# Kernel optimization log

Measured on AMD Instinct MI355X. Metric: run time of the kernel, lower is better.

Reference implementation:

```python
import jax, jax.numpy as jnp
import numpy as np

B, C, L = 16, 256, 2048


def setup_inputs() -> dict:
    key = jax.random.key(0)
    ks = jax.random.split(key, 7)
    s = 0.05
    return {
        "x": jax.random.normal(ks[0], (B, C, L), dtype=jnp.float32),
        "W_theta": jax.random.normal(ks[1], (C, C), dtype=jnp.float32) * s,
        "b_theta": jax.random.normal(ks[2], (C,), dtype=jnp.float32) * s,
        "W_phi": jax.random.normal(ks[3], (C, C), dtype=jnp.float32) * s,
        "b_phi": jax.random.normal(ks[4], (C,), dtype=jnp.float32) * s,
        "W_g": jax.random.normal(ks[5], (C, C), dtype=jnp.float32) * s,
        "b_g": jax.random.normal(ks[6], (C,), dtype=jnp.float32) * s,
    }


def reference(x, W_theta, b_theta, W_phi, b_phi, W_g, b_g):
    # x: [B, C, L]; 1x1 Conv1d == linear over channel dim: out[b,o,l] = W[o,c] x[b,c,l] + b[o]
    q = jnp.einsum('oc,bcl->bol', W_theta, x) + b_theta[None, :, None]  # [B,C,L]
    k = jnp.einsum('oc,bcl->bol', W_phi, x) + b_phi[None, :, None]
    v = jnp.einsum('oc,bcl->bol', W_g, x) + b_g[None, :, None]
    num_c = x.shape[1]
    # scores[b,i,j] = sum_c q[b,c,i] * k[b,c,j]
    scores = jnp.einsum('bci,bcj->bij', q, k) / jnp.sqrt(jnp.float32(num_c))  # [B,L,L]
    attn = jax.nn.softmax(scores, axis=-1)
    # out[b,i,c] = sum_j attn[b,i,j] v[b,c,j]; then permute back to [B,C,L]
    attn_out = jnp.einsum('bij,bcj->bci', attn, v)  # [B,C,L]
    return x + attn_out
```

## Files before the change

kernel.cpp:

```cpp
#include <hip/hip_runtime.h>
#include <math.h>

#define B_ 16
#define C_ 256
#define L_ 2048

using short8 = __attribute__((ext_vector_type(8))) short;
using f32x4  = __attribute__((ext_vector_type(4))) float;
using f32x16 = __attribute__((ext_vector_type(16))) float;
typedef unsigned int uint;

__device__ __forceinline__ unsigned short f2bf(float f) {
  unsigned u = __float_as_uint(f);
  return (unsigned short)((u + 0x7FFFu + ((u >> 16) & 1u)) >> 16);
}

__device__ __forceinline__ void gload16(const void* src, void* dst) {
  __builtin_amdgcn_global_load_lds(
      (const __attribute__((address_space(1))) unsigned int*)src,
      (__attribute__((address_space(3))) unsigned int*)dst, 16, 0, 0);
}

__global__ __launch_bounds__(256) void convert_w(const float* __restrict__ wt,
                                                 const float* __restrict__ wp,
                                                 const float* __restrict__ wg,
                                                 unsigned short* __restrict__ dst) {
  int i = blockIdx.x * 256 + threadIdx.x;
  dst[i]          = f2bf(wt[i]);
  dst[65536 + i]  = f2bf(wp[i]);
  dst[131072 + i] = f2bf(wg[i]);
}

__global__ __launch_bounds__(256, 2) void proj_kernel(
    const float* __restrict__ x, const unsigned short* __restrict__ wbf,
    const float* __restrict__ bth, const float* __restrict__ bph,
    const float* __restrict__ bg,
    unsigned short* __restrict__ qT, unsigned short* __restrict__ kT,
    unsigned short* __restrict__ vv)
{
  const int tid  = threadIdx.x;
  const int w    = tid >> 6;
  const int lane = tid & 63;
  const int r    = lane & 15;
  const int g    = lane >> 4;
  const int l0   = blockIdx.x * 64;
  const int b    = blockIdx.y;
  const int p    = blockIdx.z;

  __shared__ unsigned short xs[64 * 64];
  __shared__ unsigned short wsd[256 * 64];

  const unsigned short* wsrc = wbf + p * 65536;

  f32x4 acc[4][4];
#pragma unroll
  for (int mi = 0; mi < 4; ++mi)
#pragma unroll
    for (int ni = 0; ni < 4; ++ni) acc[mi][ni] = f32x4{0.f, 0.f, 0.f, 0.f};

  for (int ks = 0; ks < 4; ++ks) {
    __syncthreads();
#pragma unroll
    for (int it = 0; it < 8; ++it) {
      int d  = it * 256 + w * 64 + lane;
      int o  = d >> 3;
      int cs = d & 7;
      const unsigned short* src = wsrc + o * C_ + ks * 64 + ((cs ^ (o & 7)) << 3);
      gload16(src, (void*)(wsd + (size_t)(it * 256 + w * 64) * 8));
    }
#pragma unroll
    for (int it = 0; it < 16; ++it) {
      int l = (tid & 15) + 16 * (it & 3);
      int c = (tid >> 4) + 16 * (it >> 2);
      float xvv = x[((size_t)b * C_ + ks * 64 + c) * L_ + l0 + l];
      xs[l * 64 + (((c >> 3) ^ (l & 7)) << 3) + (c & 7)] = f2bf(xvv);
    }
    __syncthreads();

#pragma unroll
    for (int kk2 = 0; kk2 < 2; ++kk2) {
      short8 xf[4], wf[4];
#pragma unroll
      for (int i = 0; i < 4; ++i) {
        int lrow = 16 * i + r;
        xf[i] = *(const short8*)(xs + lrow * 64 + (((kk2 * 4 + g) ^ (lrow & 7)) << 3));
        int orow = 64 * w + 16 * i + r;
        wf[i] = *(const short8*)(wsd + orow * 64 + (((kk2 * 4 + g) ^ (orow & 7)) << 3));
      }
      if (p < 2) {
#pragma unroll
        for (int mi = 0; mi < 4; ++mi)
#pragma unroll
          for (int ni = 0; ni < 4; ++ni)
            acc[mi][ni] = __builtin_amdgcn_mfma_f32_16x16x32_bf16(xf[mi], wf[ni], acc[mi][ni], 0, 0, 0);
      } else {
#pragma unroll
        for (int mi = 0; mi < 4; ++mi)
#pragma unroll
          for (int ni = 0; ni < 4; ++ni)
            acc[mi][ni] = __builtin_amdgcn_mfma_f32_16x16x32_bf16(wf[mi], xf[ni], acc[mi][ni], 0, 0, 0);
      }
    }
  }

  if (p < 2) {
    unsigned short* dst = (p == 0) ? qT : kT;
    const float* bias   = (p == 0) ? bth : bph;
    const float scale   = (p == 0) ? 0.09016844005556021f : 1.0f;
#pragma unroll
    for (int ni = 0; ni < 4; ++ni) {
      int o    = 64 * w + 16 * ni + r;
      float bv = bias[o];
#pragma unroll
      for (int mi = 0; mi < 4; ++mi)
#pragma unroll
        for (int rr = 0; rr < 4; ++rr) {
          int l = l0 + 16 * mi + 4 * g + rr;
          dst[((size_t)b * L_ + l) * C_ + o] = f2bf((acc[mi][ni][rr] + bv) * scale);
        }
    }
  } else {
#pragma unroll
    for (int mi = 0; mi < 4; ++mi)
#pragma unroll
      for (int rr = 0; rr < 4; ++rr) {
        int o    = 64 * w + 16 * mi + 4 * g + rr;
        float bv = bg[o];
#pragma unroll
        for (int ni = 0; ni < 4; ++ni) {
          int l = l0 + 16 * ni + r;
          vv[((size_t)b * C_ + o) * L_ + l] = f2bf(acc[mi][ni][rr] + bv);
        }
      }
  }
}

__global__ __launch_bounds__(256, 2) void attn_kernel(
    const unsigned short* __restrict__ qT, const unsigned short* __restrict__ kT,
    const unsigned short* __restrict__ vv,
    const float* __restrict__ x, float* __restrict__ out)
{
  const int tid  = threadIdx.x;
  const int w    = tid >> 6;
  const int lane = tid & 63;
  const int l31  = lane & 31;
  const int hi   = lane >> 5;
  const int ih   = w >> 1;
  const int jh   = w & 1;

  int wg = ((blockIdx.x & 7) << 6) | (blockIdx.x >> 3);
  const int i0 = (wg & 31) * 64;
  const int b  = wg >> 5;

  __shared__ unsigned short kls[64 * 256];
  __shared__ unsigned short pls[64 * 64];
  __shared__ float lsums2[2][64];

  short8 qf[16];
  const unsigned short* qrow_p = qT + ((size_t)b * L_ + i0 + 32 * ih + l31) * C_;
#pragma unroll
  for (int ks = 0; ks < 16; ++ks)
    qf[ks] = *(const short8*)(qrow_p + ks * 16 + 8 * hi);

  f32x16 oacc[2][2];
#pragma unroll
  for (int it = 0; it < 2; ++it)
#pragma unroll
    for (int ct = 0; ct < 2; ++ct)
#pragma unroll
      for (int e = 0; e < 16; ++e) oacc[it][ct][e] = 0.f;
  float lsum = 0.f;

  const unsigned short* kTb = kT + (size_t)b * L_ * C_;
  const unsigned short* vvb = vv + (size_t)b * C_ * L_;

#pragma unroll
  for (int it = 0; it < 8; ++it) {
    int d   = it * 256 + w * 64 + lane;
    int row = d >> 5;
    int cs  = d & 31;
    gload16(kTb + (size_t)row * C_ + ((cs ^ (row & 7)) << 3),
            (void*)(kls + (size_t)(it * 256 + w * 64) * 8));
  }

  for (int jt = 0; jt < 32; ++jt) {
    const int j0 = jt * 64;
    __syncthreads();

    short8 vfr[2][4];
#pragma unroll
    for (int ct = 0; ct < 2; ++ct) {
      const unsigned short* vrow = vvb + (size_t)(l31 + 32 * ct + 64 * w) * L_ + j0 + 8 * hi;
#pragma unroll
      for (int ks = 0; ks < 4; ++ks)
        vfr[ct][ks] = *(const short8*)(vrow + 16 * ks);
    }

    f32x16 sacc;
#pragma unroll
    for (int e = 0; e < 16; ++e) sacc[e] = 0.f;
    const int jrow = l31 + 32 * jh;
#pragma unroll
    for (int ks = 0; ks < 16; ++ks) {
      short8 kf = *(const short8*)(kls + jrow * 256 + (((2 * ks + hi) ^ (jrow & 7)) << 3));
      sacc = __builtin_amdgcn_mfma_f32_32x32x16_bf16(kf, qf[ks], sacc, 0, 0, 0);
    }

    {
      const int i = l31 + 32 * ih;
#pragma unroll
      for (int q = 0; q < 4; ++q) {
        float p0 = exp2f(sacc[4 * q + 0]);
        float p1 = exp2f(sacc[4 * q + 1]);
        float p2 = exp2f(sacc[4 * q + 2]);
        float p3 = exp2f(sacc[4 * q + 3]);
        lsum += (p0 + p1) + (p2 + p3);
        uint2 d2;
        d2.x = (uint)f2bf(p0) | ((uint)f2bf(p1) << 16);
        d2.y = (uint)f2bf(p2) | ((uint)f2bf(p3) << 16);
        int slot = (4 * jh + q) ^ (i & 7);
        *(uint2*)(pls + i * 64 + slot * 8 + 4 * hi) = d2;
      }
    }
    __syncthreads();

    if (jt < 31) {
#pragma unroll
      for (int it = 0; it < 8; ++it) {
        int d   = it * 256 + w * 64 + lane;
        int row = d >> 5;
        int cs  = d & 31;
        gload16(kTb + (size_t)(j0 + 64 + row) * C_ + ((cs ^ (row & 7)) << 3),
                (void*)(kls + (size_t)(it * 256 + w * 64) * 8));
      }
    }

#pragma unroll
    for (int ks = 0; ks < 4; ++ks) {
      short8 pf[2];
#pragma unroll
      for (int it = 0; it < 2; ++it) {
        int irow = l31 + 32 * it;
        pf[it] = *(const short8*)(pls + irow * 64 + (((2 * ks + hi) ^ (irow & 7)) << 3));
      }
#pragma unroll
      for (int it = 0; it < 2; ++it)
#pragma unroll
        for (int ct = 0; ct < 2; ++ct)
          oacc[it][ct] = __builtin_amdgcn_mfma_f32_32x32x16_bf16(pf[it], vfr[ct][ks], oacc[it][ct], 0, 0, 0);
    }
  }

  lsum += __shfl_xor(lsum, 32);
  if (lane < 32) lsums2[jh][32 * ih + l31] = lsum;
  __syncthreads();

#pragma unroll
  for (int it = 0; it < 2; ++it)
#pragma unroll
    for (int q = 0; q < 4; ++q) {
      int ib = 32 * it + 8 * q + 4 * hi;
      f32x4 ls0 = *(const f32x4*)(&lsums2[0][ib]);
      f32x4 ls1 = *(const f32x4*)(&lsums2[1][ib]);
      f32x4 linv;
#pragma unroll
      for (int rr = 0; rr < 4; ++rr) linv[rr] = 1.0f / (ls0[rr] + ls1[rr]);
#pragma unroll
      for (int ct = 0; ct < 2; ++ct) {
        int c = l31 + 32 * ct + 64 * w;
        size_t base = ((size_t)b * C_ + c) * L_ + i0 + ib;
        f32x4 xv = *(const f32x4*)(x + base);
        f32x4 ov;
#pragma unroll
        for (int rr = 0; rr < 4; ++rr)
          ov[rr] = xv[rr] + oacc[it][ct][4 * q + rr] * linv[rr];
        *(f32x4*)(out + base) = ov;
      }
    }
}

extern "C" void kernel_launch(void* const* d_in, const int* in_sizes, int n_in,
                              void* d_out, int out_size, void* d_ws, size_t ws_size,
                              hipStream_t stream) {
  (void)in_sizes; (void)n_in; (void)out_size; (void)ws_size;
  const float* x   = (const float*)d_in[0];
  const float* wt  = (const float*)d_in[1];
  const float* bt  = (const float*)d_in[2];
  const float* wp  = (const float*)d_in[3];
  const float* bp  = (const float*)d_in[4];
  const float* wg  = (const float*)d_in[5];
  const float* bgg = (const float*)d_in[6];
  float* out = (float*)d_out;

  char* ws = (char*)d_ws;
  unsigned short* wbf = (unsigned short*)ws;
  unsigned short* qT  = (unsigned short*)(ws + 393216);
  unsigned short* kT  = (unsigned short*)(ws + 393216 + 16777216);
  unsigned short* vv  = (unsigned short*)(ws + 393216 + 2 * 16777216);

  convert_w<<<dim3(256), dim3(256), 0, stream>>>(wt, wp, wg, wbf);
  proj_kernel<<<dim3(32, 16, 3), dim3(256), 0, stream>>>(x, wbf, bt, bp, bgg, qT, kT, vv);
  attn_kernel<<<dim3(512), dim3(256), 0, stream>>>(qT, kT, vv, x, out);
}
```

Before: 147.0 us.

## Double-buffer K tiles in LDS and split score MFMA chain into two accumulators

Doubles the K tile buffer in LDS so the next tile's global-to-LDS load is issued at the top of each iteration and overlaps the QK^T and PV phases, rather than being issued after the softmax barrier. The score computation also splits its serial MFMA dependency chain into two independent accumulators that are summed before exp2, which shortens per-instruction dependency stalls. LDS use grows by 32KB per block, which may hurt occupancy at two blocks per CU, and the hand-placed waitcnt and barriers must be correct for the reuse of pls and kls.

Measured after the change: 173.7 us. 18.2% more time.

```diff
diff --git a/kernel.cpp b/kernel.cpp
--- a/kernel.cpp
+++ b/kernel.cpp
@@ -152,7 +152,7 @@
   const int i0 = (wg & 31) * 64;
   const int b  = wg >> 5;
 
-  __shared__ unsigned short kls[64 * 256];
+  __shared__ unsigned short kls[2][64 * 256];
   __shared__ unsigned short pls[64 * 64];
   __shared__ float lsums2[2][64];
 
@@ -180,12 +180,16 @@
     int row = d >> 5;
     int cs  = d & 31;
     gload16(kTb + (size_t)row * C_ + ((cs ^ (row & 7)) << 3),
-            (void*)(kls + (size_t)(it * 256 + w * 64) * 8));
+            (void*)(kls[0] + (size_t)(it * 256 + w * 64) * 8));
   }
 
   for (int jt = 0; jt < 32; ++jt) {
     const int j0 = jt * 64;
-    __syncthreads();
+    const unsigned short* kcur = kls[jt & 1];
+
+    asm volatile("s_waitcnt vmcnt(0)" ::: "memory");
+    __builtin_amdgcn_s_barrier();
+    __builtin_amdgcn_sched_barrier(0);
 
     short8 vfr[2][4];
 #pragma unroll
@@ -195,25 +199,39 @@
       for (int ks = 0; ks < 4; ++ks)
         vfr[ct][ks] = *(const short8*)(vrow + 16 * ks);
     }
-
-    f32x16 sacc;
-#pragma unroll
-    for (int e = 0; e < 16; ++e) sacc[e] = 0.f;
+    __builtin_amdgcn_sched_barrier(0);
+
+    if (jt < 31) {
+#pragma unroll
+      for (int it = 0; it < 8; ++it) {
+        int d   = it * 256 + w * 64 + lane;
+        int row = d >> 5;
+        int cs  = d & 31;
+        gload16(kTb + (size_t)(j0 + 64 + row) * C_ + ((cs ^ (row & 7)) << 3),
+                (void*)(kls[(jt + 1) & 1] + (size_t)(it * 256 + w * 64) * 8));
+      }
+    }
+
+    f32x16 sacc0, sacc1;
+#pragma unroll
+    for (int e = 0; e < 16; ++e) { sacc0[e] = 0.f; sacc1[e] = 0.f; }
     const int jrow = l31 + 32 * jh;
 #pragma unroll
-    for (int ks = 0; ks < 16; ++ks) {
-      short8 kf = *(const short8*)(kls + jrow * 256 + (((2 * ks + hi) ^ (jrow & 7)) << 3));
-      sacc = __builtin_amdgcn_mfma_f32_32x32x16_bf16(kf, qf[ks], sacc, 0, 0, 0);
+    for (int ks2 = 0; ks2 < 8; ++ks2) {
+      short8 kf0 = *(const short8*)(kcur + jrow * 256 + (((4 * ks2 + hi) ^ (jrow & 7)) << 3));
+      short8 kf1 = *(const short8*)(kcur + jrow * 256 + (((4 * ks2 + 2 + hi) ^ (jrow & 7)) << 3));
+      sacc0 = __builtin_amdgcn_mfma_f32_32x32x16_bf16(kf0, qf[2 * ks2],     sacc0, 0, 0, 0);
+      sacc1 = __builtin_amdgcn_mfma_f32_32x32x16_bf16(kf1, qf[2 * ks2 + 1], sacc1, 0, 0, 0);
     }
 
     {
       const int i = l31 + 32 * ih;
 #pragma unroll
       for (int q = 0; q < 4; ++q) {
-        float p0 = exp2f(sacc[4 * q + 0]);
-        float p1 = exp2f(sacc[4 * q + 1]);
-        float p2 = exp2f(sacc[4 * q + 2]);
-        float p3 = exp2f(sacc[4 * q + 3]);
+        float p0 = exp2f(sacc0[4 * q + 0] + sacc1[4 * q + 0]);
+        float p1 = exp2f(sacc0[4 * q + 1] + sacc1[4 * q + 1]);
+        float p2 = exp2f(sacc0[4 * q + 2] + sacc1[4 * q + 2]);
+        float p3 = exp2f(sacc0[4 * q + 3] + sacc1[4 * q + 3]);
         lsum += (p0 + p1) + (p2 + p3);
         uint2 d2;
         d2.x = (uint)f2bf(p0) | ((uint)f2bf(p1) << 16);
@@ -222,18 +240,10 @@
         *(uint2*)(pls + i * 64 + slot * 8 + 4 * hi) = d2;
       }
     }
-    __syncthreads();
-
-    if (jt < 31) {
-#pragma unroll
-      for (int it = 0; it < 8; ++it) {
-        int d   = it * 256 + w * 64 + lane;
-        int row = d >> 5;
-        int cs  = d & 31;
-        gload16(kTb + (size_t)(j0 + 64 + row) * C_ + ((cs ^ (row & 7)) << 3),
-                (void*)(kls + (size_t)(it * 256 + w * 64) * 8));
-      }
-    }
+
+    asm volatile("s_waitcnt lgkmcnt(0)" ::: "memory");
+    __builtin_amdgcn_s_barrier();
+    __builtin_amdgcn_sched_barrier(0);
 
 #pragma unroll
     for (int ks = 0; ks < 4; ++ks) {
```
